# Performance work log

Hardware: AMD Instinct MI355X
Metric: run time of the kernel (lower is better)

Reference implementation:

```python
import jax, jax.numpy as jnp
import numpy as np

# c_val = 1.0 fixed by init_kwargs
C = 1.0
SQC = 1.0  # sqrt(c)
EPS = 1e-5  # atanh clamp for numerical stability

def _norm(x):
    return jnp.sqrt(jnp.sum(x * x, axis=-1, keepdims=True))

def _atanh(x):
    return jnp.arctanh(jnp.clip(x, -1.0 + EPS, 1.0 - EPS))

def _project(x, eps=1e-5):
    # clip to Poincare ball of radius (1-eps)/sqrt(c)
    max_norm = (1.0 - eps) / SQC
    n = _norm(x)
    return jnp.where(n > max_norm, x * (max_norm / (n + 1e-10)), x)

def _exp0(v):
    # exponential map at origin
    n = jnp.maximum(_norm(v), 1e-10)
    return jnp.tanh(SQC * n) * v / (SQC * n)

def _log0(y):
    # logarithmic map at origin
    n = jnp.maximum(_norm(y), 1e-10)
    return _atanh(SQC * n) * y / (SQC * n)

def _mob_add(u, v):
    # Mobius addition u (+)_c v
    uv = jnp.sum(u * v, axis=-1, keepdims=True)
    u2 = jnp.sum(u * u, axis=-1, keepdims=True)
    v2 = jnp.sum(v * v, axis=-1, keepdims=True)
    num = (1.0 + 2.0 * C * uv + C * v2) * u + (1.0 - C * u2) * v
    den = 1.0 + 2.0 * C * uv + C * C * u2 * v2
    return num / (den + 1e-10)

def _mob_matmul(x, M):
    # Mobius matrix-vector multiply: x [B,d] hyperbolic, M [d,k]
    mx = x @ M
    xn = jnp.maximum(_norm(x), 1e-10)
    mxn = jnp.maximum(_norm(mx), 1e-10)
    return jnp.tanh(mxn / xn * _atanh(SQC * xn)) * mx / (mxn * SQC)

def _mob_pw(v, u):
    # Mobius pointwise (diagonal) product: v hyperbolic, u euclidean gate
    mx = v * u
    vn = jnp.maximum(_norm(v), 1e-10)
    mxn = jnp.maximum(_norm(mx), 1e-10)
    return jnp.tanh(mxn / vn * _atanh(SQC * vn)) * mx / (mxn * SQC)

def _one_transform(W, h, U, x, b):
    # bias_geom == 'hyp' -> bias used directly
    res = _mob_add(_mob_add(_mob_matmul(h, W), _mob_matmul(x, U)), b)
    return _project(res, eps=1e-5)

def setup_inputs() -> dict:
    key = jax.random.key(0)
    ks = jax.random.split(key, 8)
    B, D, H = 16384, 1024, 1024
    def xav(k, fi, fo):
        s = (2.0 / (fi + fo)) ** 0.5
        return jax.random.normal(k, (fi, fo), jnp.float32) * s
    return {
        "inputs": jax.random.normal(ks[0], (B, D), jnp.float32),
        "state": jax.random.normal(ks[1], (B, H), jnp.float32) * 0.1,
        "Wz": xav(ks[2], H, H), "Uz": xav(ks[3], D, H), "bz": jnp.zeros((1, H), jnp.float32),
        "Wr": xav(ks[4], H, H), "Ur": xav(ks[5], D, H), "br": jnp.zeros((1, H), jnp.float32),
        "Wh": xav(ks[6], H, H), "Uh": xav(ks[7], D, H), "bh": jnp.zeros((1, H), jnp.float32),
    }

def reference(inputs, state, Wz, Uz, bz, Wr, Ur, br, Wh, Uh, bh):
    state = _project(state, eps=1e-4)
    hyp_x = _exp0(inputs)  # inputs_geom == 'eucl'
    # gates: sigmoid in tangent space (hyp_output=False)
    z = jax.nn.sigmoid(_log0(_one_transform(Wz, state, Uz, hyp_x, bz)))
    r = jax.nn.sigmoid(_log0(_one_transform(Wr, state, Ur, hyp_x, br)))
    r_point_h = _project(_mob_pw(state, r), eps=1e-4)
    # non_lin == 'id', hyp_output=True -> identity
    h_tilde = _project(_one_transform(Wh, r_point_h, Uh, hyp_x, bh), eps=1e-4)
    minus_h_oplus_htilde = _mob_add(-state, h_tilde)
    update_step = _mob_pw(minus_h_oplus_htilde, z)
    new_h = _project(_mob_add(state, update_step), eps=1e-5)
    return new_h
```

## Files before the change

### kernel.cpp

```cpp
#include <hip/hip_runtime.h>
#include <math.h>

typedef unsigned short u16;
typedef __attribute__((ext_vector_type(8))) short bf16x8;
typedef __attribute__((ext_vector_type(4))) float f32x4;

#define DHID 1024

__device__ __forceinline__ u16 f2bf(float f) {
  union { float f; unsigned u; } v; v.f = f;
  unsigned u = v.u;
  u = (u + 0x7fffu + ((u >> 16) & 1u)) >> 16;
  return (u16)u;
}
__device__ __forceinline__ float bf2f(u16 h) {
  union { unsigned u; float f; } v; v.u = ((unsigned)h) << 16;
  return v.f;
}
__device__ __forceinline__ float wred(float v) {
  #pragma unroll
  for (int m = 32; m > 0; m >>= 1) v += __shfl_xor(v, m, 64);
  return v;
}
__device__ __forceinline__ float frcp(float x) { return __builtin_amdgcn_rcpf(x); }
__device__ __forceinline__ float ftanh(float x) {
  x = fminf(fmaxf(x, -15.f), 15.f);
  float t = __expf(2.f * x);
  return (t - 1.f) * frcp(t + 1.f);
}
__device__ __forceinline__ float fatanh(float x) {
  x = fminf(fmaxf(x, -1.0f + 1e-5f), 1.0f - 1e-5f);
  return 0.5f * __logf((1.f + x) * frcp(1.f - x));
}
__device__ __forceinline__ float fsig(float x) {
  return frcp(1.f + __expf(-x));
}

struct W6 { const float* s[6]; u16* d[6]; };
__global__ __launch_bounds__(256) void wconv_all(W6 p) {
  const float* __restrict__ src = p.s[blockIdx.z];
  u16* __restrict__ dst = p.d[blockIdx.z];
  __shared__ float t[32][33];
  int bx = blockIdx.x * 32, by = blockIdx.y * 32;
  int tx = threadIdx.x, ty = threadIdx.y;
  #pragma unroll
  for (int r = 0; r < 32; r += 8)
    t[ty + r][tx] = src[(size_t)(by + ty + r) * DHID + bx + tx];
  __syncthreads();
  #pragma unroll
  for (int r = 0; r < 32; r += 8)
    dst[(size_t)(bx + ty + r) * DHID + by + tx] = f2bf(t[tx][ty + r]);
}

__global__ __launch_bounds__(256) void prep(const float* __restrict__ x, const float* __restrict__ h,
    u16* __restrict__ xb, u16* __restrict__ hb, float* __restrict__ nx, float* __restrict__ nh, int B) {
  int row = blockIdx.x * 4 + (threadIdx.x >> 6);
  if (row >= B) return;
  int lane = threadIdx.x & 63;
  size_t base = (size_t)row * DHID;
  const float4* xr = (const float4*)(x + base);
  const float4* hr = (const float4*)(h + base);
  ushort4* xo = (ushort4*)(xb + base);
  ushort4* ho = (ushort4*)(hb + base);
  float sx = 0.f, sh = 0.f;
  #pragma unroll
  for (int j = 0; j < 4; ++j) {
    int idx = j * 64 + lane;
    float4 a = xr[idx], b = hr[idx];
    sx += a.x*a.x + a.y*a.y + a.z*a.z + a.w*a.w;
    sh += b.x*b.x + b.y*b.y + b.z*b.z + b.w*b.w;
    xo[idx] = make_ushort4(f2bf(a.x), f2bf(a.y), f2bf(a.z), f2bf(a.w));
    ho[idx] = make_ushort4(f2bf(b.x), f2bf(b.y), f2bf(b.z), f2bf(b.w));
  }
  sx = wred(sx); sh = wred(sh);
  if (lane == 0) { nx[row] = sqrtf(sx); nh[row] = sqrtf(sh); }
}

__device__ __forceinline__ void gll16(const void* g, void* l) {
  __builtin_amdgcn_global_load_lds((const __attribute__((address_space(1))) unsigned int*)g,
                                   (__attribute__((address_space(3))) unsigned int*)l, 16, 0, 0);
}

struct GB { const u16* A[4]; const u16* Bt[4]; u16* C[4]; };
__global__ __launch_bounds__(256) void gemm_bf16(GB gb, int M, int N, int K) {
  const u16* __restrict__ A  = gb.A[blockIdx.z];
  const u16* __restrict__ Bt = gb.Bt[blockIdx.z];
  u16* __restrict__ C        = gb.C[blockIdx.z];
  __shared__ __align__(16) u16 As[128 * 64];
  __shared__ __align__(16) u16 Bs[128 * 64];
  const int tid = threadIdx.x;
  const int lane = tid & 63;
  const int wid = tid >> 6;
  const int wr = (wid >> 1) * 64;
  const int wc = (wid & 1) * 64;
  const int l15 = lane & 15;
  const int koff = (lane >> 4) * 8;
  const int cswz = (l15 & 7) << 3;
  const int srow = lane >> 3;
  const int scol = ((lane & 7) ^ srow) * 8;
  const size_t abase = (size_t)(blockIdx.x * 128) * K;
  const size_t bbase = (size_t)(blockIdx.y * 128) * K;
  f32x4 acc[4][4] = {};
  for (int k0 = 0; k0 < K; k0 += 64) {
    __syncthreads();
    #pragma unroll
    for (int i = 0; i < 4; ++i) {
      int rb = (i * 4 + wid) * 8;
      gll16(A  + abase + (size_t)(rb + srow) * K + k0 + scol, &As[rb * 64]);
      gll16(Bt + bbase + (size_t)(rb + srow) * K + k0 + scol, &Bs[rb * 64]);
    }
    __syncthreads();
    #pragma unroll
    for (int ks = 0; ks < 64; ks += 32) {
      bf16x8 af[4], bg[4];
      #pragma unroll
      for (int m = 0; m < 4; ++m)
        af[m] = *(const bf16x8*)&As[(wr + m*16 + l15) * 64 + ((ks + koff) ^ cswz)];
      #pragma unroll
      for (int n = 0; n < 4; ++n)
        bg[n] = *(const bf16x8*)&Bs[(wc + n*16 + l15) * 64 + ((ks + koff) ^ cswz)];
      #pragma unroll
      for (int m = 0; m < 4; ++m)
        #pragma unroll
        for (int n = 0; n < 4; ++n)
          acc[m][n] = __builtin_amdgcn_mfma_f32_16x16x32_bf16(af[m], bg[n], acc[m][n], 0, 0, 0);
    }
  }
  const int r4 = (lane >> 4) * 4;
  #pragma unroll
  for (int m = 0; m < 4; ++m)
    #pragma unroll
    for (int n = 0; n < 4; ++n) {
      size_t col = (size_t)blockIdx.y * 128 + wc + n * 16 + l15;
      #pragma unroll
      for (int j = 0; j < 4; ++j) {
        size_t row = (size_t)blockIdx.x * 128 + wr + m * 16 + r4 + j;
        C[row * N + col] = f2bf(acc[m][n][j]);
      }
    }
}

__device__ __forceinline__ void load_bf16_row(const u16* p, int lane, float v[16]) {
  #pragma unroll
  for (int j = 0; j < 4; ++j) {
    int idx = j * 64 + lane;
    ushort4 a = ((const ushort4*)p)[idx];
    v[4*j+0] = bf2f(a.x); v[4*j+1] = bf2f(a.y); v[4*j+2] = bf2f(a.z); v[4*j+3] = bf2f(a.w);
  }
}
__device__ __forceinline__ void load_f32_row(const float* p, int lane, float v[16]) {
  #pragma unroll
  for (int j = 0; j < 4; ++j) {
    int idx = j * 64 + lane;
    float4 a = ((const float4*)p)[idx];
    v[4*j+0] = a.x; v[4*j+1] = a.y; v[4*j+2] = a.z; v[4*j+3] = a.w;
  }
}

struct RowCtx {
  float scale_h, hnc, ath, scale_x, xn, atx;
};

__device__ __forceinline__ RowCtx make_ctx(float n_h, float n_x) {
  RowCtx c;
  c.scale_h = (n_h > 0.9999f) ? 0.9999f * frcp(n_h + 1e-10f) : 1.0f;
  float hn = n_h * c.scale_h;
  c.hnc = fmaxf(hn, 1e-10f);
  c.ath = fatanh(hn);
  float nxc = fmaxf(n_x, 1e-10f);
  c.scale_x = ftanh(nxc) * frcp(nxc);
  c.xn = fmaxf(n_x * c.scale_x, 1e-10f);
  c.atx = fatanh(c.xn);
  return c;
}

__device__ __forceinline__ void gate_sig(const float gh[16], const float gx[16], const float bb[16],
                                         const RowCtx& c, float out[16], float sv[16]) {
  float sh = 0.f, sx = 0.f, dxy = 0.f;
  #pragma unroll
  for (int j = 0; j < 16; ++j) { sh += gh[j]*gh[j]; sx += gx[j]*gx[j]; dxy += gh[j]*gx[j]; }
  sh = wred(sh); sx = wred(sx); dxy = wred(dxy);
  float mhn = fmaxf(c.scale_h * sqrtf(sh), 1e-10f);
  float th  = ftanh(mhn * frcp(c.hnc) * c.ath);
  float ca  = th * c.scale_h * frcp(mhn);
  float mxn = fmaxf(c.scale_x * sqrtf(sx), 1e-10f);
  float tx  = ftanh(mxn * frcp(c.xn) * c.atx);
  float cb  = tx * c.scale_x * frcp(mxn);
  float uv = ca * cb * dxy;
  float u2 = th * th, v2 = tx * tx;
  float rden = frcp(1.f + 2.f*uv + u2*v2 + 1e-10f);
  float c1 = (1.f + 2.f*uv + v2) * rden * ca;
  float c2 = (1.f - u2) * rden * cb;
  float uvb = 0.f, u2s = 0.f, v2b = 0.f;
  #pragma unroll
  for (int j = 0; j < 16; ++j) {
    sv[j] = c1 * gh[j] + c2 * gx[j];
    uvb += sv[j] * bb[j]; u2s += sv[j] * sv[j]; v2b += bb[j] * bb[j];
  }
  uvb = wred(uvb); u2s = wred(u2s); v2b = wred(v2b);
  float rden2 = frcp(1.f + 2.f*uvb + u2s*v2b + 1e-10f);
  float d1 = (1.f + 2.f*uvb + v2b) * rden2, d2 = (1.f - u2s) * rden2;
  float s3 = 0.f;
  #pragma unroll
  for (int j = 0; j < 16; ++j) { sv[j] = d1 * sv[j] + d2 * bb[j]; s3 += sv[j]*sv[j]; }
  s3 = wred(s3);
  float ns = sqrtf(s3);
  float ps = (ns > 0.99999f) ? 0.99999f * frcp(ns + 1e-10f) : 1.0f;
  float nres = fmaxf(ns * ps, 1e-10f);
  float g = fatanh(nres) * frcp(nres) * ps;
  #pragma unroll
  for (int j = 0; j < 16; ++j) out[j] = fsig(g * sv[j]);
}

__global__ __launch_bounds__(256) void gates_k(
    const u16* __restrict__ Gzh, const u16* __restrict__ Gzx,
    const u16* __restrict__ Grh, const u16* __restrict__ Grx,
    const float* __restrict__ state, const float* __restrict__ bz, const float* __restrict__ br,
    const float* __restrict__ nxA, const float* __restrict__ nhA,
    float* __restrict__ zout, u16* __restrict__ rphb, float* __restrict__ rnA, int B) {
  int row = blockIdx.x * 4 + (threadIdx.x >> 6);
  if (row >= B) return;
  int lane = threadIdx.x & 63;
  size_t base = (size_t)row * DHID;
  RowCtx c = make_ctx(nhA[row], nxA[row]);

  float gh[16], gx[16], bb[16], st[16], out[16], sv[16];
  load_f32_row(state + base, lane, st);

  load_bf16_row(Gzh + base, lane, gh);
  load_bf16_row(Gzx + base, lane, gx);
  load_f32_row(bz, lane, bb);
  gate_sig(gh, gx, bb, c, out, sv);
  #pragma unroll
  for (int j = 0; j < 4; ++j) {
    int idx = j * 64 + lane;
    ((float4*)(zout + base))[idx] = make_float4(out[4*j], out[4*j+1], out[4*j+2], out[4*j+3]);
  }

  load_bf16_row(Grh + base, lane, gh);
  load_bf16_row(Grx + base, lane, gx);
  load_f32_row(br, lane, bb);
  gate_sig(gh, gx, bb, c, out, sv);

  float mxv[16]; float s = 0.f;
  #pragma unroll
  for (int j = 0; j < 16; ++j) { mxv[j] = st[j] * c.scale_h * out[j]; s += mxv[j]*mxv[j]; }
  s = wred(s);
  float mxn = fmaxf(sqrtf(s), 1e-10f);
  float t = ftanh(mxn * frcp(c.hnc) * c.ath);
  float cc = t * frcp(mxn);
  float nrp = t;
  float psc = (nrp > 0.9999f) ? 0.9999f * frcp(nrp + 1e-10f) : 1.0f;
  cc *= psc; nrp *= psc;
  #pragma unroll
  for (int j = 0; j < 4; ++j) {
    int idx = j * 64 + lane;
    ((ushort4*)(rphb + base))[idx] = make_ushort4(
        f2bf(cc*mxv[4*j+0]), f2bf(cc*mxv[4*j+1]), f2bf(cc*mxv[4*j+2]), f2bf(cc*mxv[4*j+3]));
  }
  if (lane == 0) rnA[row] = nrp;
}

__global__ __launch_bounds__(256) void final_k(
    const u16* __restrict__ Ghh, const u16* __restrict__ Ghx,
    const float* __restrict__ state, const float* __restrict__ bh,
    const float* __restrict__ nxA, const float* __restrict__ nhA, const float* __restrict__ rnA,
    float* __restrict__ io, int B) {
  int row = blockIdx.x * 4 + (threadIdx.x >> 6);
  if (row >= B) return;
  int lane = threadIdx.x & 63;
  size_t base = (size_t)row * DHID;
  float n_h = nhA[row], n_x = nxA[row], rn = rnA[row];
  float scale_h = (n_h > 0.9999f) ? 0.9999f * frcp(n_h + 1e-10f) : 1.0f;
  float hn = n_h * scale_h;
  float nxc = fmaxf(n_x, 1e-10f);
  float scale_x = ftanh(nxc) * frcp(nxc);
  float xn = fmaxf(n_x * scale_x, 1e-10f);
  float atx = fatanh(xn);
  float hna = fmaxf(rn, 1e-10f);
  float atr = fatanh(rn);

  float gh[16], gx[16], bb[16], st[16], zz[16], sv[16];
  load_f32_row(state + base, lane, st);
  load_f32_row(io + base, lane, zz);
  load_bf16_row(Ghh + base, lane, gh);
  load_bf16_row(Ghx + base, lane, gx);
  load_f32_row(bh, lane, bb);

  float sh = 0.f, sx = 0.f, dxy = 0.f;
  #pragma unroll
  for (int j = 0; j < 16; ++j) { sh += gh[j]*gh[j]; sx += gx[j]*gx[j]; dxy += gh[j]*gx[j]; }
  sh = wred(sh); sx = wred(sx); dxy = wred(dxy);
  float mhn = fmaxf(sqrtf(sh), 1e-10f);
  float ta = ftanh(mhn * frcp(hna) * atr);
  float ca = ta * frcp(mhn);
  float mxn = fmaxf(scale_x * sqrtf(sx), 1e-10f);
  float tb = ftanh(mxn * frcp(xn) * atx);
  float cb = tb * scale_x * frcp(mxn);
  float uv = ca * cb * dxy;
  float u2 = ta * ta, v2 = tb * tb;
  float rden = frcp(1.f + 2.f*uv + u2*v2 + 1e-10f);
  float c1 = (1.f + 2.f*uv + v2) * rden * ca;
  float c2 = (1.f - u2) * rden * cb;
  float uvb = 0.f, u2s = 0.f, v2b = 0.f;
  #pragma unroll
  for (int j = 0; j < 16; ++j) {
    sv[j] = c1 * gh[j] + c2 * gx[j];
    uvb += sv[j]*bb[j]; u2s += sv[j]*sv[j]; v2b += bb[j]*bb[j];
  }
  uvb = wred(uvb); u2s = wred(u2s); v2b = wred(v2b);
  float rden2 = frcp(1.f + 2.f*uvb + u2s*v2b + 1e-10f);
  float d1 = (1.f + 2.f*uvb + v2b) * rden2, d2 = (1.f - u2s) * rden2;
  float s3 = 0.f;
  #pragma unroll
  for (int j = 0; j < 16; ++j) { sv[j] = d1 * sv[j] + d2 * bb[j]; s3 += sv[j]*sv[j]; }
  s3 = wred(s3);
  float ns = sqrtf(s3);
  float p1 = (ns > 0.99999f) ? 0.99999f * frcp(ns + 1e-10f) : 1.0f;
  float n1 = ns * p1;
  float p2 = (n1 > 0.9999f) ? 0.9999f * frcp(n1 + 1e-10f) : 1.0f;
  float pc = p1 * p2;
  float nht = n1 * p2;
  #pragma unroll
  for (int j = 0; j < 16; ++j) sv[j] *= pc;

  float dv = 0.f;
  #pragma unroll
  for (int j = 0; j < 16; ++j) dv += st[j] * sv[j];
  dv = wred(dv);
  float uv2 = -scale_h * dv;
  float u2m = hn * hn, v2m = nht * nht;
  float rden3 = frcp(1.f + 2.f*uv2 + u2m*v2m + 1e-10f);
  float e1 = -(1.f + 2.f*uv2 + v2m) * rden3 * scale_h;
  float e2 = (1.f - u2m) * rden3;
  float mv[16]; float sm = 0.f;
  #pragma unroll
  for (int j = 0; j < 16; ++j) { mv[j] = e1*st[j] + e2*sv[j]; sm += mv[j]*mv[j]; }
  sm = wred(sm);
  float vn = fmaxf(sqrtf(sm), 1e-10f);
  float atv = fatanh(vn);
  float mx2[16]; float s4 = 0.f;
  #pragma unroll
  for (int j = 0; j < 16; ++j) { mx2[j] = mv[j]*zz[j]; s4 += mx2[j]*mx2[j]; }
  s4 = wred(s4);
  float mxn2 = fmaxf(sqrtf(s4), 1e-10f);
  float tu = ftanh(mxn2 * frcp(vn) * atv);
  float cu2 = tu * frcp(mxn2);
  float d5 = 0.f;
  #pragma unroll
  for (int j = 0; j < 16; ++j) d5 += st[j]*mx2[j];
  d5 = wred(d5);
  float uv3 = scale_h * cu2 * d5;
  float u2f = hn * hn, v2f = tu * tu;
  float rden4 = frcp(1.f + 2.f*uv3 + u2f*v2f + 1e-10f);
  float f1 = (1.f + 2.f*uv3 + v2f) * rden4 * scale_h;
  float f2 = (1.f - u2f) * rden4 * cu2;
  float nh4[16]; float s5 = 0.f;
  #pragma unroll
  for (int j = 0; j < 16; ++j) { nh4[j] = f1*st[j] + f2*mx2[j]; s5 += nh4[j]*nh4[j]; }
  s5 = wred(s5);
  float nf = sqrtf(s5);
  float pf = (nf > 0.99999f) ? 0.99999f * frcp(nf + 1e-10f) : 1.0f;
  #pragma unroll
  for (int j = 0; j < 4; ++j) {
    int idx = j * 64 + lane;
    ((float4*)(io + base))[idx] = make_float4(pf*nh4[4*j], pf*nh4[4*j+1], pf*nh4[4*j+2], pf*nh4[4*j+3]);
  }
}

extern "C" void kernel_launch(void* const* d_in, const int* in_sizes, int n_in,
                              void* d_out, int out_size, void* d_ws, size_t ws_size,
                              hipStream_t stream) {
  const float* inputs = (const float*)d_in[0];
  const float* state  = (const float*)d_in[1];
  const float* Wz = (const float*)d_in[2];
  const float* Uz = (const float*)d_in[3];
  const float* bz = (const float*)d_in[4];
  const float* Wr = (const float*)d_in[5];
  const float* Ur = (const float*)d_in[6];
  const float* br = (const float*)d_in[7];
  const float* Wh = (const float*)d_in[8];
  const float* Uh = (const float*)d_in[9];
  const float* bh = (const float*)d_in[10];
  const int B = in_sizes[0] / DHID;
  const size_t MD = (size_t)B * DHID;

  char* p = (char*)d_ws;
  u16* xb = (u16*)p;  p += MD * 2;
  u16* hb = (u16*)p;  p += MD * 2;
  u16* Wt0 = (u16*)p; p += (size_t)DHID*DHID*2;
  u16* Wt1 = (u16*)p; p += (size_t)DHID*DHID*2;
  u16* Wt2 = (u16*)p; p += (size_t)DHID*DHID*2;
  u16* Wt3 = (u16*)p; p += (size_t)DHID*DHID*2;
  u16* Wt4 = (u16*)p; p += (size_t)DHID*DHID*2;
  u16* Wt5 = (u16*)p; p += (size_t)DHID*DHID*2;
  u16* G0 = (u16*)p;  p += MD * 2;
  u16* G1 = (u16*)p;  p += MD * 2;
  u16* G2 = (u16*)p;  p += MD * 2;
  u16* G3 = (u16*)p;  p += MD * 2;
  float* nx = (float*)p; p += (size_t)B * 4;
  float* nh = (float*)p; p += (size_t)B * 4;
  float* rn = (float*)p; p += (size_t)B * 4;
  if ((size_t)(p - (char*)d_ws) > ws_size) return;

  float* zbuf = (float*)d_out;

  prep<<<B/4, 256, 0, stream>>>(inputs, state, xb, hb, nx, nh, B);

  W6 wp;
  wp.s[0] = Wz; wp.s[1] = Wr; wp.s[2] = Wh; wp.s[3] = Uz; wp.s[4] = Ur; wp.s[5] = Uh;
  wp.d[0] = Wt0; wp.d[1] = Wt1; wp.d[2] = Wt2; wp.d[3] = Wt3; wp.d[4] = Wt4; wp.d[5] = Wt5;
  dim3 tb(32, 8), tg(DHID/32, DHID/32, 6);
  wconv_all<<<tg, tb, 0, stream>>>(wp);

  GB g1;
  g1.A[0] = hb; g1.Bt[0] = Wt0; g1.C[0] = G0;
  g1.A[1] = hb; g1.Bt[1] = Wt1; g1.C[1] = G1;
  g1.A[2] = xb; g1.Bt[2] = Wt3; g1.C[2] = G2;
  g1.A[3] = xb; g1.Bt[3] = Wt4; g1.C[3] = G3;
  dim3 gg1(B/128, DHID/128, 4);
  gemm_bf16<<<gg1, 256, 0, stream>>>(g1, B, DHID, DHID);

  gates_k<<<B/4, 256, 0, stream>>>(G0, G2, G1, G3, state, bz, br, nx, nh, zbuf, hb, rn, B);

  GB g2;
  g2.A[0] = hb; g2.Bt[0] = Wt2; g2.C[0] = G0;
  g2.A[1] = xb; g2.Bt[1] = Wt5; g2.C[1] = G1;
  g2.A[2] = hb; g2.Bt[2] = Wt2; g2.C[2] = G0;
  g2.A[3] = xb; g2.Bt[3] = Wt5; g2.C[3] = G1;
  dim3 gg2(B/128, DHID/128, 2);
  gemm_bf16<<<gg2, 256, 0, stream>>>(g2, B, DHID, DHID);

  final_k<<<B/4, 256, 0, stream>>>(G0, G1, state, bh, nx, nh, rn, zbuf, B);
}
```

Measured before the change: 393.6 us.

## Concatenate gate weights into wide GEMMs and store z gate in bf16 scratch

Concatenates the z and r gate weight matrices so the first GEMM computes both gates in a single N=2048 output per input, and swaps grid axes so blocks sharing an A row tile run together. The z gate is stored as bf16 in the unused half of the gate buffer instead of fp32 in the output buffer, and gates_k reads state from the bf16 copy rather than fp32. This reduces global memory traffic and improves L2 reuse, at the cost of extra bf16 rounding on z and state in the gate path.

```diff
diff --git a/kernel.cpp b/kernel.cpp
--- a/kernel.cpp
+++ b/kernel.cpp
@@ -81,8 +81,8 @@
                                    (__attribute__((address_space(3))) unsigned int*)l, 16, 0, 0);
 }
 
-struct GB { const u16* A[4]; const u16* Bt[4]; u16* C[4]; };
-__global__ __launch_bounds__(256) void gemm_bf16(GB gb, int M, int N, int K) {
+struct GB { const u16* A[2]; const u16* Bt[2]; u16* C[2]; };
+__global__ __launch_bounds__(256) void gemm_bf16(GB gb, int K, int ldC) {
   const u16* __restrict__ A  = gb.A[blockIdx.z];
   const u16* __restrict__ Bt = gb.Bt[blockIdx.z];
   u16* __restrict__ C        = gb.C[blockIdx.z];
@@ -98,8 +98,8 @@
   const int cswz = (l15 & 7) << 3;
   const int srow = lane >> 3;
   const int scol = ((lane & 7) ^ srow) * 8;
-  const size_t abase = (size_t)(blockIdx.x * 128) * K;
-  const size_t bbase = (size_t)(blockIdx.y * 128) * K;
+  const size_t abase = (size_t)(blockIdx.y * 128) * K;
+  const size_t bbase = (size_t)(blockIdx.x * 128) * K;
   f32x4 acc[4][4] = {};
   for (int k0 = 0; k0 < K; k0 += 64) {
     __syncthreads();
@@ -131,11 +131,11 @@
   for (int m = 0; m < 4; ++m)
     #pragma unroll
     for (int n = 0; n < 4; ++n) {
-      size_t col = (size_t)blockIdx.y * 128 + wc + n * 16 + l15;
+      size_t col = (size_t)blockIdx.x * 128 + wc + n * 16 + l15;
       #pragma unroll
       for (int j = 0; j < 4; ++j) {
-        size_t row = (size_t)blockIdx.x * 128 + wr + m * 16 + r4 + j;
-        C[row * N + col] = f2bf(acc[m][n][j]);
+        size_t row = (size_t)blockIdx.y * 128 + wr + m * 16 + r4 + j;
+        C[row * ldC + col] = f2bf(acc[m][n][j]);
       }
     }
 }
@@ -213,34 +213,40 @@
 }
 
 __global__ __launch_bounds__(256) void gates_k(
-    const u16* __restrict__ Gzh, const u16* __restrict__ Gzx,
-    const u16* __restrict__ Grh, const u16* __restrict__ Grx,
-    const float* __restrict__ state, const float* __restrict__ bz, const float* __restrict__ br,
+    u16* G01, const u16* __restrict__ G23,
+    u16* hbuf,
+    const float* __restrict__ bz, const float* __restrict__ br,
     const float* __restrict__ nxA, const float* __restrict__ nhA,
-    float* __restrict__ zout, u16* __restrict__ rphb, float* __restrict__ rnA, int B) {
+    float* __restrict__ rnA, int B) {
   int row = blockIdx.x * 4 + (threadIdx.x >> 6);
   if (row >= B) return;
   int lane = threadIdx.x & 63;
-  size_t base = (size_t)row * DHID;
+  size_t base  = (size_t)row * DHID;
+  size_t base2 = (size_t)row * 2048;
   RowCtx c = make_ctx(nhA[row], nxA[row]);
 
   float gh[16], gx[16], bb[16], st[16], out[16], sv[16];
-  load_f32_row(state + base, lane, st);
-
-  load_bf16_row(Gzh + base, lane, gh);
-  load_bf16_row(Gzx + base, lane, gx);
+  load_bf16_row(hbuf + base, lane, st);
+
+  load_bf16_row(G01 + base2, lane, gh);
+  load_bf16_row(G23 + base2, lane, gx);
   load_f32_row(bz, lane, bb);
   gate_sig(gh, gx, bb, c, out, sv);
-  #pragma unroll
-  for (int j = 0; j < 4; ++j) {
-    int idx = j * 64 + lane;
-    ((float4*)(zout + base))[idx] = make_float4(out[4*j], out[4*j+1], out[4*j+2], out[4*j+3]);
-  }
-
-  load_bf16_row(Grh + base, lane, gh);
-  load_bf16_row(Grx + base, lane, gx);
+  float zo[16];
+  #pragma unroll
+  for (int j = 0; j < 16; ++j) zo[j] = out[j];
+
+  load_bf16_row(G01 + base2 + DHID, lane, gh);
+  load_bf16_row(G23 + base2 + DHID, lane, gx);
   load_f32_row(br, lane, bb);
   gate_sig(gh, gx, bb, c, out, sv);
+
+  #pragma unroll
+  for (int j = 0; j < 4; ++j) {
+    int idx = j * 64 + lane;
+    ((ushort4*)(G01 + base2 + DHID))[idx] = make_ushort4(
+        f2bf(zo[4*j+0]), f2bf(zo[4*j+1]), f2bf(zo[4*j+2]), f2bf(zo[4*j+3]));
+  }
 
   float mxv[16]; float s = 0.f;
   #pragma unroll
@@ -255,21 +261,22 @@
   #pragma unroll
   for (int j = 0; j < 4; ++j) {
     int idx = j * 64 + lane;
-    ((ushort4*)(rphb + base))[idx] = make_ushort4(
+    ((ushort4*)(hbuf + base))[idx] = make_ushort4(
         f2bf(cc*mxv[4*j+0]), f2bf(cc*mxv[4*j+1]), f2bf(cc*mxv[4*j+2]), f2bf(cc*mxv[4*j+3]));
   }
   if (lane == 0) rnA[row] = nrp;
 }
 
 __global__ __launch_bounds__(256) void final_k(
-    const u16* __restrict__ Ghh, const u16* __restrict__ Ghx,
+    const u16* __restrict__ G01, const u16* __restrict__ G23,
     const float* __restrict__ state, const float* __restrict__ bh,
     const float* __restrict__ nxA, const float* __restrict__ nhA, const float* __restrict__ rnA,
-    float* __restrict__ io, int B) {
+    float* __restrict__ out, int B) {
   int row = blockIdx.x * 4 + (threadIdx.x >> 6);
   if (row >= B) return;
   int lane = threadIdx.x & 63;
-  size_t base = (size_t)row * DHID;
+  size_t base  = (size_t)row * DHID;
+  size_t base2 = (size_t)row * 2048;
   float n_h = nhA[row], n_x = nxA[row], rn = rnA[row];
   float scale_h = (n_h > 0.9999f) ? 0.9999f * frcp(n_h + 1e-10f) : 1.0f;
   float hn = n_h * scale_h;
@@ -282,9 +289,9 @@
 
   float gh[16], gx[16], bb[16], st[16], zz[16], sv[16];
   load_f32_row(state + base, lane, st);
-  load_f32_row(io + base, lane, zz);
-  load_bf16_row(Ghh + base, lane, gh);
-  load_bf16_row(Ghx + base, lane, gx);
+  load_bf16_row(G01 + base2 + DHID, lane, zz);
+  load_bf16_row(G01 + base2, lane, gh);
+  load_bf16_row(G23 + base2, lane, gx);
   load_f32_row(bh, lane, bb);
 
   float sh = 0.f, sx = 0.f, dxy = 0.f;
@@ -364,7 +371,7 @@
   #pragma unroll
   for (int j = 0; j < 4; ++j) {
     int idx = j * 64 + lane;
-    ((float4*)(io + base))[idx] = make_float4(pf*nh4[4*j], pf*nh4[4*j+1], pf*nh4[4*j+2], pf*nh4[4*j+3]);
+    ((float4*)(out + base))[idx] = make_float4(pf*nh4[4*j], pf*nh4[4*j+1], pf*nh4[4*j+2], pf*nh4[4*j+3]);
   }
 }
 
@@ -384,52 +391,44 @@
   const float* bh = (const float*)d_in[10];
   const int B = in_sizes[0] / DHID;
   const size_t MD = (size_t)B * DHID;
+  const size_t WD = (size_t)DHID * DHID;
 
   char* p = (char*)d_ws;
-  u16* xb = (u16*)p;  p += MD * 2;
-  u16* hb = (u16*)p;  p += MD * 2;
-  u16* Wt0 = (u16*)p; p += (size_t)DHID*DHID*2;
-  u16* Wt1 = (u16*)p; p += (size_t)DHID*DHID*2;
-  u16* Wt2 = (u16*)p; p += (size_t)DHID*DHID*2;
-  u16* Wt3 = (u16*)p; p += (size_t)DHID*DHID*2;
-  u16* Wt4 = (u16*)p; p += (size_t)DHID*DHID*2;
-  u16* Wt5 = (u16*)p; p += (size_t)DHID*DHID*2;
-  u16* G0 = (u16*)p;  p += MD * 2;
-  u16* G1 = (u16*)p;  p += MD * 2;
-  u16* G2 = (u16*)p;  p += MD * 2;
-  u16* G3 = (u16*)p;  p += MD * 2;
+  u16* xb   = (u16*)p; p += MD * 2;
+  u16* hb   = (u16*)p; p += MD * 2;
+  u16* Wt01 = (u16*)p; p += WD * 2 * 2;
+  u16* Wt34 = (u16*)p; p += WD * 2 * 2;
+  u16* Wt2  = (u16*)p; p += WD * 2;
+  u16* Wt5  = (u16*)p; p += WD * 2;
+  u16* G01  = (u16*)p; p += MD * 2 * 2;
+  u16* G23  = (u16*)p; p += MD * 2 * 2;
   float* nx = (float*)p; p += (size_t)B * 4;
   float* nh = (float*)p; p += (size_t)B * 4;
   float* rn = (float*)p; p += (size_t)B * 4;
   if ((size_t)(p - (char*)d_ws) > ws_size) return;
 
-  float* zbuf = (float*)d_out;
-
   prep<<<B/4, 256, 0, stream>>>(inputs, state, xb, hb, nx, nh, B);
 
   W6 wp;
-  wp.s[0] = Wz; wp.s[1] = Wr; wp.s[2] = Wh; wp.s[3] = Uz; wp.s[4] = Ur; wp.s[5] = Uh;
-  wp.d[0] = Wt0; wp.d[1] = Wt1; wp.d[2] = Wt2; wp.d[3] = Wt3; wp.d[4] = Wt4; wp.d[5] = Wt5;
+  wp.s[0] = Wz; wp.s[1] = Wr; wp.s[2] = Uz; wp.s[3] = Ur; wp.s[4] = Wh; wp.s[5] = Uh;
+  wp.d[0] = Wt01; wp.d[1] = Wt01 + WD; wp.d[2] = Wt34; wp.d[3] = Wt34 + WD;
+  wp.d[4] = Wt2;  wp.d[5] = Wt5;
   dim3 tb(32, 8), tg(DHID/32, DHID/32, 6);
   wconv_all<<<tg, tb, 0, stream>>>(wp);
 
   GB g1;
-  g1.A[0] = hb; g1.Bt[0] = Wt0; g1.C[0] = G0;
-  g1.A[1] = hb; g1.Bt[1] = Wt1; g1.C[1] = G1;
-  g1.A[2] = xb; g1.Bt[2] = Wt3; g1.C[2] = G2;
-  g1.A[3] = xb; g1.Bt[3] = Wt4; g1.C[3] = G3;
-  dim3 gg1(B/128, DHID/128, 4);
-  gemm_bf16<<<gg1, 256, 0, stream>>>(g1, B, DHID, DHID);
-
-  gates_k<<<B/4, 256, 0, stream>>>(G0, G2, G1, G3, state, bz, br, nx, nh, zbuf, hb, rn, B);
+  g1.A[0] = hb; g1.Bt[0] = Wt01; g1.C[0] = G01;
+  g1.A[1] = xb; g1.Bt[1] = Wt34; g1.C[1] = G23;
+  dim3 gg1(2*DHID/128, B/128, 2);
+  gemm_bf16<<<gg1, 256, 0, stream>>>(g1, DHID, 2*DHID);
+
+  gates_k<<<B/4, 256, 0, stream>>>(G01, G23, hb, bz, br, nx, nh, rn, B);
 
   GB g2;
-  g2.A[0] = hb; g2.Bt[0] = Wt2; g2.C[0] = G0;
-  g2.A[1] = xb; g2.Bt[1] = Wt5; g2.C[1] = G1;
-  g2.A[2] = hb; g2.Bt[2] = Wt2; g2.C[2] = G0;
-  g2.A[3] = xb; g2.Bt[3] = Wt5; g2.C[3] = G1;
-  dim3 gg2(B/128, DHID/128, 2);
-  gemm_bf16<<<gg2, 256, 0, stream>>>(g2, B, DHID, DHID);
-
-  final_k<<<B/4, 256, 0, stream>>>(G0, G1, state, bh, nx, nh, rn, zbuf, B);
-}
+  g2.A[0] = hb; g2.Bt[0] = Wt2; g2.C[0] = G01;
+  g2.A[1] = xb; g2.Bt[1] = Wt5; g2.C[1] = G23;
+  dim3 gg2(DHID/128, B/128, 2);
+  gemm_bf16<<<gg2, 256, 0, stream>>>(g2, DHID, 2*DHID);
+
+  final_k<<<B/4, 256, 0, stream>>>(G01, G23, state, bh, nx, nh, rn, (float*)d_out, B);
+}
```

Measured after the change: 382.4 us. 1.03x faster.
